# Performance work log

Hardware: AMD Instinct MI355X
Metric: run time of the kernel (lower is better)

Reference implementation:

```python
import jax, jax.numpy as jnp
import numpy as np

N = 50000
E = 600000
IN_C = 128
HID_C = 128
OUT_C = 128


def _glorot(key, shape):
    fan_in, fan_out = shape[0], shape[1]
    lim = np.sqrt(6.0 / (fan_in + fan_out))
    return jax.random.uniform(key, shape, jnp.float32, -lim, lim)


def setup_inputs() -> dict:
    key = jax.random.key(0)
    ks = jax.random.split(key, 10)
    x = jax.random.normal(ks[0], (N, IN_C), jnp.float32)
    edge_index = jax.random.randint(ks[1], (2, E), 0, N, jnp.int64)
    return {
        "x": x,
        "edge_index": edge_index,
        # SAGEConv1: lin_l (aggregated, with bias) and lin_r (root, no bias)
        "W1_l": _glorot(ks[2], (IN_C, HID_C)),
        "b1_l": jnp.zeros((HID_C,), jnp.float32),
        "W1_r": _glorot(ks[3], (IN_C, HID_C)),
        # SAGEConv2
        "W2_l": _glorot(ks[4], (HID_C, OUT_C)),
        "b2_l": jnp.zeros((OUT_C,), jnp.float32),
        "W2_r": _glorot(ks[5], (HID_C, OUT_C)),
        # final Linear(hidden+out -> out)
        "W_lin": _glorot(ks[6], (HID_C + OUT_C, OUT_C)),
        "b_lin": jnp.zeros((OUT_C,), jnp.float32),
    }


def _sage_conv(x, src, dst, W_l, b_l, W_r):
    # mean-aggregate source features onto destination nodes
    msg = x[src]                                   # [E, C] gather
    agg = jax.ops.segment_sum(msg, dst, num_segments=N)        # [N, C]
    cnt = jax.ops.segment_sum(jnp.ones((src.shape[0],), x.dtype), dst,
                              num_segments=N)                   # [N]
    mean = agg / jnp.maximum(cnt, 1.0)[:, None]
    return mean @ W_l + b_l + x @ W_r


def reference(x, edge_index, W1_l, b1_l, W1_r, W2_l, b2_l, W2_r, W_lin, b_lin):
    src, dst = edge_index[0], edge_index[1]
    x1 = jax.nn.relu(_sage_conv(x, src, dst, W1_l, b1_l, W1_r))   # [N, HID]
    x2 = jax.nn.relu(_sage_conv(x1, src, dst, W2_l, b2_l, W2_r))  # [N, OUT]
    return jnp.concatenate([x1, x2], axis=-1) @ W_lin + b_lin     # [N, OUT]
```

## Files before the change

kernel.cpp:

```cpp
#include <hip/hip_runtime.h>


typedef _Float16 f16;
typedef __attribute__((ext_vector_type(4))) _Float16 f16x4;
typedef __attribute__((ext_vector_type(8))) _Float16 f16x8;
typedef __attribute__((ext_vector_type(4))) float f32x4;

__global__ void prep_kernel(const float* __restrict__ x, f16* __restrict__ xh, int n4,
                            const int* __restrict__ ei, int* __restrict__ deg, int E,
                            const float* __restrict__ W1l, const float* __restrict__ W1r,
                            const float* __restrict__ W2l, const float* __restrict__ W2r,
                            const float* __restrict__ Wlin, f16* __restrict__ wt,
                            int cb, int db) {
  int b = blockIdx.x;
  if (b < cb) {
    int i = b * 256 + threadIdx.x;
    if (i < n4) {
      const float4 v = ((const float4*)x)[i];
      f16x4 h = { (f16)v.x, (f16)v.y, (f16)v.z, (f16)v.w };
      ((f16x4*)xh)[i] = h;
    }
  } else if (b < cb + db) {
    int e = (b - cb) * 256 + threadIdx.x;
    if (e < E) atomicAdd(&deg[ei[E + e]], 1);
  } else {
    int tid = (b - cb - db) * 256 + threadIdx.x;
    int w = tid >> 15, idx = tid & 32767;
    int j = idx & 7, n = (idx >> 3) & 127, chunk = idx >> 10;
    int k = chunk * 8 + j;
    float v;
    if (w == 0) v = (k < 128) ? W1l[k * 128 + n] : W1r[(k - 128) * 128 + n];
    else if (w == 1) v = (k < 128) ? W2l[k * 128 + n] : W2r[(k - 128) * 128 + n];
    else v = Wlin[k * 128 + n];
    wt[tid] = (f16)v;
  }
}

__global__ void scan_block_kernel(const int* __restrict__ in, int* __restrict__ out,
                                  int* __restrict__ sums, int n) {
  __shared__ int s[2][1024];
  int t = threadIdx.x;
  int gid = blockIdx.x * 1024 + t;
  int v = (gid < n) ? in[gid] : 0;
  int cur = 0;
  s[0][t] = v;
  __syncthreads();
  for (int ofs = 1; ofs < 1024; ofs <<= 1) {
    int nv = s[cur][t] + ((t >= ofs) ? s[cur][t - ofs] : 0);
    s[cur ^ 1][t] = nv;
    cur ^= 1;
    __syncthreads();
  }
  if (gid < n) out[gid] = s[cur][t] - v;
  if (t == 1023) sums[blockIdx.x] = s[cur][1023];
}

__global__ void scan_add_kernel(int* __restrict__ off, const int* __restrict__ sums,
                                int* __restrict__ cur, int n, int E) {
  __shared__ int prefix_s;
  int b = blockIdx.x;
  if (threadIdx.x < 64) {
    int v = ((int)threadIdx.x < b) ? sums[threadIdx.x] : 0;
#pragma unroll
    for (int ofs = 1; ofs < 64; ofs <<= 1) v += __shfl_xor(v, ofs);
    if (threadIdx.x == 0) prefix_s = v;
  }
  __syncthreads();
  int gid = b * 1024 + threadIdx.x;
  if (gid < n) { off[gid] += prefix_s; cur[gid] = 0; }
  if (gid == 0) off[n] = E;
}

__global__ void fill_kernel(const int* __restrict__ ei, const int* __restrict__ off,
                            int* __restrict__ cursor, int* __restrict__ srcs, int E) {
  int e = blockIdx.x * blockDim.x + threadIdx.x;
  if (e < E) {
    int src = ei[e], dst = ei[E + e];
    int pos = atomicAdd(&cursor[dst], 1);
    srcs[off[dst] + pos] = src;
  }
}

#define AGG_R 6
__global__ void aggregate_kernel(const f16* __restrict__ feat, const int* __restrict__ off,
                                 const int* __restrict__ srcs, f16* __restrict__ meanf, int n) {
  int pair = (int)((blockIdx.x * blockDim.x + threadIdx.x) >> 6);
  int w0 = pair * 2;
  if (w0 >= n) return;
  int w1 = w0 + 1;
  int lane = threadIdx.x & 63;
  int sub = lane >> 4, n15 = lane & 15;
  int beg0 = off[w0], end0 = off[w0 + 1];
  int beg1 = end0;
  int end1 = (w1 < n) ? off[w1 + 1] : end0;
  int deg0 = end0 - beg0, deg1 = end1 - beg1;

  int s0[AGG_R], s1[AGG_R];
  bool v0[AGG_R], v1[AGG_R];
#pragma unroll
  for (int k = 0; k < AGG_R; ++k) {
    int p = 4 * k + sub;
    v0[k] = p < deg0;  s0[k] = v0[k] ? srcs[beg0 + p] : 0;
    v1[k] = p < deg1;  s1[k] = v1[k] ? srcs[beg1 + p] : 0;
  }
  f16x8 g0[AGG_R], g1[AGG_R];
#pragma unroll
  for (int k = 0; k < AGG_R; ++k) {
    if (v0[k]) g0[k] = *(const f16x8*)(feat + (size_t)s0[k] * 128 + n15 * 8);
    if (v1[k]) g1[k] = *(const f16x8*)(feat + (size_t)s1[k] * 128 + n15 * 8);
  }
  float acc0[8] = {}, acc1[8] = {};
#pragma unroll
  for (int k = 0; k < AGG_R; ++k) {
    if (v0[k]) {
#pragma unroll
      for (int j = 0; j < 8; ++j) acc0[j] += (float)g0[k][j];
    }
    if (v1[k]) {
#pragma unroll
      for (int j = 0; j < 8; ++j) acc1[j] += (float)g1[k][j];
    }
  }
  for (int e = beg0 + 4 * AGG_R; e < end0; e += 4) {
    if (sub < end0 - e) {
      int s = srcs[e + sub];
      f16x8 g = *(const f16x8*)(feat + (size_t)s * 128 + n15 * 8);
#pragma unroll
      for (int j = 0; j < 8; ++j) acc0[j] += (float)g[j];
    }
  }
  for (int e = beg1 + 4 * AGG_R; e < end1; e += 4) {
    if (sub < end1 - e) {
      int s = srcs[e + sub];
      f16x8 g = *(const f16x8*)(feat + (size_t)s * 128 + n15 * 8);
#pragma unroll
      for (int j = 0; j < 8; ++j) acc1[j] += (float)g[j];
    }
  }
#pragma unroll
  for (int j = 0; j < 8; ++j) {
    acc0[j] += __shfl_xor(acc0[j], 16);
    acc0[j] += __shfl_xor(acc0[j], 32);
    acc1[j] += __shfl_xor(acc1[j], 16);
    acc1[j] += __shfl_xor(acc1[j], 32);
  }
  if (sub == 0) {
    float inv = 1.0f / fmaxf((float)deg0, 1.0f);
    f16x8 o;
#pragma unroll
    for (int j = 0; j < 8; ++j) o[j] = (f16)(acc0[j] * inv);
    *(f16x8*)(meanf + (size_t)w0 * 128 + n15 * 8) = o;
  } else if (sub == 1 && w1 < n) {
    float inv = 1.0f / fmaxf((float)deg1, 1.0f);
    f16x8 o;
#pragma unroll
    for (int j = 0; j < 8; ++j) o[j] = (f16)(acc1[j] * inv);
    *(f16x8*)(meanf + (size_t)w1 * 128 + n15 * 8) = o;
  }
}

template <bool RELU, bool OUT16>
__global__ __launch_bounds__(256, 4) void gemm_kernel(
    const f16* __restrict__ U, const f16* __restrict__ V, const f16* __restrict__ Wt,
    const float* __restrict__ bias, void* __restrict__ outp, int M) {
  __shared__ f16 ldsb[16384];
  int tid = threadIdx.x;
  int wave = tid >> 6, lane = tid & 63;
  int quad = lane >> 4, n15 = lane & 15;
  int bx = blockIdx.x >> 1, ch = blockIdx.x & 1;
  int m0 = bx * 128 + wave * 32;
  int kq = quad * 8;

  f16x8 a[2][8];
#pragma unroll
  for (int r = 0; r < 2; ++r) {
    int row = m0 + r * 16 + n15;
    int rowc = row < M ? row : M - 1;
    const f16* bu = U + (size_t)rowc * 128 + kq;
    const f16* bv = V + (size_t)rowc * 128 + kq;
#pragma unroll
    for (int kk = 0; kk < 4; ++kk) a[r][kk] = *(const f16x8*)(bu + kk * 32);
#pragma unroll
    for (int kk = 4; kk < 8; ++kk) a[r][kk] = *(const f16x8*)(bv + (kk - 4) * 32);
  }

#pragma unroll
  for (int it = 0; it < 8; ++it) {
    int g = it * 256 + tid;
    int chunk = g >> 6, w64 = g & 63;
    ((f16x8*)ldsb)[g] = ((const f16x8*)Wt)[chunk * 128 + ch * 64 + w64];
  }
  __syncthreads();

  f32x4 acc[2][4] = {};
#pragma unroll
  for (int kk = 0; kk < 8; ++kk) {
#pragma unroll
    for (int t = 0; t < 4; ++t) {
      f16x8 b = ((const f16x8*)ldsb)[(kk * 4 + quad) * 64 + t * 16 + n15];
#pragma unroll
      for (int r = 0; r < 2; ++r)
        acc[r][t] = __builtin_amdgcn_mfma_f32_16x16x32_f16(a[r][kk], b, acc[r][t], 0, 0, 0);
    }
  }

  int rbase0 = m0 + quad * 4;
#pragma unroll
  for (int t = 0; t < 4; ++t) {
    int col = ch * 64 + t * 16 + n15;
    float bv = bias[col];
#pragma unroll
    for (int r = 0; r < 2; ++r) {
#pragma unroll
      for (int i = 0; i < 4; ++i) {
        int row = rbase0 + r * 16 + i;
        if (row < M) {
          float v = acc[r][t][i] + bv;
          if (RELU) v = fmaxf(v, 0.f);
          size_t idx = (size_t)row * 128 + col;
          if (OUT16) ((f16*)outp)[idx] = (f16)v;
          else       ((float*)outp)[idx] = v;
        }
      }
    }
  }
}

extern "C" void kernel_launch(void* const* d_in, const int* in_sizes, int n_in,
                              void* d_out, int out_size, void* d_ws, size_t ws_size,
                              hipStream_t stream) {
  (void)n_in; (void)out_size; (void)ws_size;
  const float* x    = (const float*)d_in[0];
  const int*   ei   = (const int*)d_in[1];
  const float* W1l  = (const float*)d_in[2];
  const float* b1l  = (const float*)d_in[3];
  const float* W1r  = (const float*)d_in[4];
  const float* W2l  = (const float*)d_in[5];
  const float* b2l  = (const float*)d_in[6];
  const float* W2r  = (const float*)d_in[7];
  const float* Wlin = (const float*)d_in[8];
  const float* blin = (const float*)d_in[9];
  const int N = in_sizes[0] / 128;
  const int E = in_sizes[1] / 2;

  char* ws = (char*)d_ws;
  size_t o = 0;
  auto alloc = [&](size_t bytes) {
    char* p = ws + o;
    o = (o + bytes + 255) & ~(size_t)255;
    return p;
  };
  f16* xh   = (f16*)alloc((size_t)N * 128 * 2);
  f16* x1h  = (f16*)alloc((size_t)N * 128 * 2);
  f16* x2h  = (f16*)alloc((size_t)N * 128 * 2);
  f16* mh   = (f16*)alloc((size_t)N * 128 * 2);
  f16* wt   = (f16*)alloc((size_t)3 * 32768 * 2);
  int* deg  = (int*)alloc((size_t)N * 4);
  int* cur  = (int*)alloc((size_t)N * 4);
  int* off  = (int*)alloc(((size_t)N + 1) * 4);
  int* srcs = (int*)alloc((size_t)E * 4);
  int* sums = (int*)alloc(64 * 4);
  f16* wt1 = wt, *wt2 = wt + 32768, *wt3 = wt + 65536;

  hipMemsetAsync(deg, 0, (size_t)N * 4, stream);

  const int n4 = N * 128 / 4;
  const int cb = (n4 + 255) / 256;
  const int db = (E + 255) / 256;
  const int wb = (3 * 32768) / 256;
  prep_kernel<<<cb + db + wb, 256, 0, stream>>>(x, xh, n4, ei, deg, E,
                                                W1l, W1r, W2l, W2r, Wlin, wt, cb, db);

  const int nb = (N + 1023) / 1024;
  scan_block_kernel<<<nb, 1024, 0, stream>>>(deg, off, sums, N);
  scan_add_kernel<<<nb, 1024, 0, stream>>>(off, sums, cur, N, E);
  fill_kernel<<<db, 256, 0, stream>>>(ei, off, cur, srcs, E);

  const int aggBlocks  = ((N + 1) / 2 + 3) / 4;
  const int gemmBlocks = 2 * ((N + 127) / 128);

  aggregate_kernel<<<aggBlocks, 256, 0, stream>>>(xh, off, srcs, mh, N);
  gemm_kernel<true, true><<<gemmBlocks, 256, 0, stream>>>(mh, xh, wt1, b1l, x1h, N);
  aggregate_kernel<<<aggBlocks, 256, 0, stream>>>(x1h, off, srcs, mh, N);
  gemm_kernel<true, true><<<gemmBlocks, 256, 0, stream>>>(mh, x1h, wt2, b2l, x2h, N);
  gemm_kernel<false, false><<<gemmBlocks, 256, 0, stream>>>(x1h, x2h, wt3, blin, d_out, N);
}
```

Baseline: 264.8 us.

## Build CSR with two-pass LDS radix sort instead of global atomics

```diff
diff --git a/kernel.cpp b/kernel.cpp
--- a/kernel.cpp
+++ b/kernel.cpp
@@ -6,12 +6,13 @@
 typedef __attribute__((ext_vector_type(8))) _Float16 f16x8;
 typedef __attribute__((ext_vector_type(4))) float f32x4;
 
+#define RNB 128
+
 __global__ void prep_kernel(const float* __restrict__ x, f16* __restrict__ xh, int n4,
-                            const int* __restrict__ ei, int* __restrict__ deg, int E,
                             const float* __restrict__ W1l, const float* __restrict__ W1r,
                             const float* __restrict__ W2l, const float* __restrict__ W2r,
                             const float* __restrict__ Wlin, f16* __restrict__ wt,
-                            int cb, int db) {
+                            int cb) {
   int b = blockIdx.x;
   if (b < cb) {
     int i = b * 256 + threadIdx.x;
@@ -20,11 +21,8 @@
       f16x4 h = { (f16)v.x, (f16)v.y, (f16)v.z, (f16)v.w };
       ((f16x4*)xh)[i] = h;
     }
-  } else if (b < cb + db) {
-    int e = (b - cb) * 256 + threadIdx.x;
-    if (e < E) atomicAdd(&deg[ei[E + e]], 1);
   } else {
-    int tid = (b - cb - db) * 256 + threadIdx.x;
+    int tid = (b - cb) * 256 + threadIdx.x;
     int w = tid >> 15, idx = tid & 32767;
     int j = idx & 7, n = (idx >> 3) & 127, chunk = idx >> 10;
     int k = chunk * 8 + j;
@@ -36,6 +34,18 @@
   }
 }
 
+__global__ void radix_hist(const int* __restrict__ ei, int* __restrict__ ghist, int E) {
+  __shared__ int h[256];
+  int tid = threadIdx.x, b = blockIdx.x;
+  h[tid] = 0;
+  __syncthreads();
+  int per = (E + RNB - 1) / RNB;
+  int s = b * per, e = s + per; if (e > E) e = E;
+  for (int i = s + tid; i < e; i += 256) atomicAdd(&h[ei[E + i] >> 8], 1);
+  __syncthreads();
+  ghist[tid * RNB + b] = h[tid];
+}
+
 __global__ void scan_block_kernel(const int* __restrict__ in, int* __restrict__ out,
                                   int* __restrict__ sums, int n) {
   __shared__ int s[2][1024];
@@ -55,8 +65,7 @@
   if (t == 1023) sums[blockIdx.x] = s[cur][1023];
 }
 
-__global__ void scan_add_kernel(int* __restrict__ off, const int* __restrict__ sums,
-                                int* __restrict__ cur, int n, int E) {
+__global__ void scan_add_kernel(int* __restrict__ data, const int* __restrict__ sums, int n) {
   __shared__ int prefix_s;
   int b = blockIdx.x;
   if (threadIdx.x < 64) {
@@ -67,17 +76,53 @@
   }
   __syncthreads();
   int gid = b * 1024 + threadIdx.x;
-  if (gid < n) { off[gid] += prefix_s; cur[gid] = 0; }
-  if (gid == 0) off[n] = E;
-}
-
-__global__ void fill_kernel(const int* __restrict__ ei, const int* __restrict__ off,
-                            int* __restrict__ cursor, int* __restrict__ srcs, int E) {
-  int e = blockIdx.x * blockDim.x + threadIdx.x;
-  if (e < E) {
-    int src = ei[e], dst = ei[E + e];
-    int pos = atomicAdd(&cursor[dst], 1);
-    srcs[off[dst] + pos] = src;
+  if (gid < n) data[gid] += prefix_s;
+}
+
+__global__ void radix_scatter(const int* __restrict__ ei, const int* __restrict__ sg,
+                              int2* __restrict__ tmp, int E) {
+  __shared__ int cur[256];
+  int tid = threadIdx.x, b = blockIdx.x;
+  cur[tid] = sg[tid * RNB + b];
+  __syncthreads();
+  int per = (E + RNB - 1) / RNB;
+  int s = b * per, e = s + per; if (e > E) e = E;
+  for (int i = s + tid; i < e; i += 256) {
+    int d = ei[E + i], sr = ei[i];
+    int pos = atomicAdd(&cur[d >> 8], 1);
+    tmp[pos] = make_int2(d, sr);
+  }
+}
+
+__global__ void radix_bucket(const int2* __restrict__ tmp, const int* __restrict__ sg,
+                             int* __restrict__ srcs, int* __restrict__ off,
+                             int N, int E, int HB) {
+  __shared__ int h[256], sc[256], cur[256];
+  int tid = threadIdx.x, hb = blockIdx.x;
+  int start = sg[hb * RNB];
+  int end = (hb + 1 < HB) ? sg[(hb + 1) * RNB] : E;
+  h[tid] = 0;
+  __syncthreads();
+  for (int i = start + tid; i < end; i += 256) atomicAdd(&h[tmp[i].x & 255], 1);
+  __syncthreads();
+  sc[tid] = h[tid];
+  __syncthreads();
+  for (int o = 1; o < 256; o <<= 1) {
+    int u = (tid >= o) ? sc[tid - o] : 0;
+    __syncthreads();
+    sc[tid] += u;
+    __syncthreads();
+  }
+  int excl = sc[tid] - h[tid];
+  int v = (hb << 8) + tid;
+  if (v < N) off[v] = start + excl;
+  if (hb == 0 && tid == 0) off[N] = E;
+  cur[tid] = start + excl;
+  __syncthreads();
+  for (int i = start + tid; i < end; i += 256) {
+    int2 p = tmp[i];
+    int pos = atomicAdd(&cur[p.x & 255], 1);
+    srcs[pos] = p.y;
   }
 }
 
@@ -250,31 +295,33 @@
     o = (o + bytes + 255) & ~(size_t)255;
     return p;
   };
-  f16* xh   = (f16*)alloc((size_t)N * 128 * 2);
-  f16* x1h  = (f16*)alloc((size_t)N * 128 * 2);
-  f16* x2h  = (f16*)alloc((size_t)N * 128 * 2);
-  f16* mh   = (f16*)alloc((size_t)N * 128 * 2);
-  f16* wt   = (f16*)alloc((size_t)3 * 32768 * 2);
-  int* deg  = (int*)alloc((size_t)N * 4);
-  int* cur  = (int*)alloc((size_t)N * 4);
-  int* off  = (int*)alloc(((size_t)N + 1) * 4);
-  int* srcs = (int*)alloc((size_t)E * 4);
-  int* sums = (int*)alloc(64 * 4);
+  f16*  xh   = (f16*)alloc((size_t)N * 128 * 2);
+  f16*  x1h  = (f16*)alloc((size_t)N * 128 * 2);
+  f16*  x2h  = (f16*)alloc((size_t)N * 128 * 2);
+  f16*  mh   = (f16*)alloc((size_t)N * 128 * 2);
+  f16*  wt   = (f16*)alloc((size_t)3 * 32768 * 2);
+  int*  off  = (int*)alloc(((size_t)N + 1) * 4);
+  int*  srcs = (int*)alloc((size_t)E * 4);
+  int2* tmp  = (int2*)alloc((size_t)E * 8);
+  int*  ghist= (int*)alloc(256 * RNB * 4);
+  int*  sg   = (int*)alloc(256 * RNB * 4);
+  int*  sums = (int*)alloc(64 * 4);
   f16* wt1 = wt, *wt2 = wt + 32768, *wt3 = wt + 65536;
-
-  hipMemsetAsync(deg, 0, (size_t)N * 4, stream);
 
   const int n4 = N * 128 / 4;
   const int cb = (n4 + 255) / 256;
-  const int db = (E + 255) / 256;
   const int wb = (3 * 32768) / 256;
-  prep_kernel<<<cb + db + wb, 256, 0, stream>>>(x, xh, n4, ei, deg, E,
-                                                W1l, W1r, W2l, W2r, Wlin, wt, cb, db);
-
-  const int nb = (N + 1023) / 1024;
-  scan_block_kernel<<<nb, 1024, 0, stream>>>(deg, off, sums, N);
-  scan_add_kernel<<<nb, 1024, 0, stream>>>(off, sums, cur, N, E);
-  fill_kernel<<<db, 256, 0, stream>>>(ei, off, cur, srcs, E);
+  const int HB = (N + 255) / 256;
+  const int SN = 256 * RNB;
+  const int snb = SN / 1024;
+
+  radix_hist<<<RNB, 256, 0, stream>>>(ei, ghist, E);
+  scan_block_kernel<<<snb, 1024, 0, stream>>>(ghist, sg, sums, SN);
+  scan_add_kernel<<<snb, 1024, 0, stream>>>(sg, sums, SN);
+  radix_scatter<<<RNB, 256, 0, stream>>>(ei, sg, tmp, E);
+  radix_bucket<<<HB, 256, 0, stream>>>(tmp, sg, srcs, off, N, E, HB);
+
+  prep_kernel<<<cb + wb, 256, 0, stream>>>(x, xh, n4, W1l, W1r, W2l, W2r, Wlin, wt, cb);
 
   const int aggBlocks  = ((N + 1) / 2 + 3) / 4;
   const int gemmBlocks = 2 * ((N + 127) / 128);
```

After: 229.0 us. 1.16x faster.
